# Kernel tuning notes

Hardware: AMD Instinct MI355X
Metric: run time of the kernel (lower is better)

The kernel has to match this reference:

```python
import jax, jax.numpy as jnp
import numpy as np

N_NODES = 200000
N_EDGES = 3200000
F_IN = 128
CH = 32
N_GRAPHS = 1024
N_LABELS = 17


def setup_inputs() -> dict:
    key = jax.random.key(0)
    ks = jax.random.split(key, 16)
    x = jax.random.normal(ks[0], (N_NODES, F_IN), dtype=jnp.float32)
    a_row = jax.random.randint(ks[1], (N_EDGES,), 0, N_NODES, dtype=jnp.int64)
    a_col = jax.random.randint(ks[2], (N_EDGES,), 0, N_NODES, dtype=jnp.int64)
    a_val = jax.random.uniform(ks[3], (N_EDGES,), dtype=jnp.float32)
    seg = jnp.sort(jax.random.randint(ks[4], (N_NODES,), 0, N_GRAPHS, dtype=jnp.int64))
    def glorot(k, fan_in, fan_out):
        lim = np.sqrt(6.0 / (fan_in + fan_out)).astype(np.float32)
        return jax.random.uniform(k, (fan_in, fan_out), dtype=jnp.float32, minval=-lim, maxval=lim)
    params = {
        'W1_1': glorot(ks[5], F_IN, CH), 'W2_1': glorot(ks[6], F_IN, CH), 'b_1': jnp.zeros((CH,), jnp.float32),
        'W1_2': glorot(ks[7], CH, CH),   'W2_2': glorot(ks[8], CH, CH),   'b_2': jnp.zeros((CH,), jnp.float32),
        'W1_3': glorot(ks[9], CH, CH),   'W2_3': glorot(ks[10], CH, CH),  'b_3': jnp.zeros((CH,), jnp.float32),
        'Wd': glorot(ks[11], CH, N_LABELS), 'bd': jnp.zeros((N_LABELS,), jnp.float32),
    }
    return dict(x=x, a_row=a_row, a_col=a_col, a_val=a_val, seg=seg, **params)


def _gcs_conv(x, a_row, a_col, a_val, W1, W2, b):
    # A @ X via gather(col) -> weight -> scatter-add(row)
    msgs = a_val[:, None] * x[a_col]            # [E, F]
    agg = jax.ops.segment_sum(msgs, a_row, num_segments=N_NODES)  # [N, F]
    return jax.nn.relu(agg @ W1 + x @ W2 + b)


def reference(x, a_row, a_col, a_val, seg,
              W1_1, W2_1, b_1, W1_2, W2_2, b_2, W1_3, W2_3, b_3, Wd, bd):
    h = _gcs_conv(x, a_row, a_col, a_val, W1_1, W2_1, b_1)
    h = _gcs_conv(h, a_row, a_col, a_val, W1_2, W2_2, b_2)
    h = _gcs_conv(h, a_row, a_col, a_val, W1_3, W2_3, b_3)
    # GlobalAvgPool over batch index i: segment mean per graph
    sums = jax.ops.segment_sum(h, seg, num_segments=N_GRAPHS)          # [G, CH]
    cnts = jax.ops.segment_sum(jnp.ones((N_NODES,), h.dtype), seg, num_segments=N_GRAPHS)
    pooled = sums / jnp.maximum(cnts, 1.0)[:, None]
    return jax.nn.softmax(pooled @ Wd + bd, axis=-1)
```

## Files before the change

kernel.cpp:

```cpp
#include <hip/hip_runtime.h>
#include <cstdint>

#define N_NODES 200000
#define N_EDGES 3200000
#define F_IN 128
#define CH 32
#define N_GRAPHS 1024
#define N_LABELS 17

#define BROWS 512
#define NBUCK ((N_NODES + BROWS - 1) / BROWS)
#define CAP 10240
#define EPB 8192

typedef unsigned int uint32;
typedef unsigned short u16;

#define TSCALE 16.f

__device__ __forceinline__ u16 f2bf(float f) {
  unsigned int u = __float_as_uint(f);
  u = (u + 0x7FFFu + ((u >> 16) & 1u)) >> 16;
  return (u16)u;
}
__device__ __forceinline__ float bf2f(u16 h) {
  return __uint_as_float(((unsigned int)h) << 16);
}
__device__ __forceinline__ signed char f2q8(float f) {
  float qf = fmaxf(-127.f, fminf(127.f, rintf(f * TSCALE)));
  return (signed char)(int)qf;
}


__global__ __launch_bounds__(256) void k_passA(const int* __restrict__ arow,
                                               const int* __restrict__ acol,
                                               const float* __restrict__ aval,
                                               int* __restrict__ bucketCur,
                                               unsigned long long* __restrict__ records) {
  __shared__ int cnt[NBUCK];
  __shared__ int base[NBUCK];
  int t = threadIdx.x;
  for (int i = t; i < NBUCK; i += 256) cnt[i] = 0;
  __syncthreads();
  int e0 = blockIdx.x * EPB;
  int e1 = e0 + EPB; if (e1 > N_EDGES) e1 = N_EDGES;
  for (int e = e0 + t; e < e1; e += 256) atomicAdd(&cnt[arow[e] >> 9], 1);
  __syncthreads();
  for (int i = t; i < NBUCK; i += 256) {
    int n = cnt[i];
    base[i] = n ? atomicAdd(&bucketCur[i], n) : 0;
    cnt[i] = 0;
  }
  __syncthreads();
  for (int e = e0 + t; e < e1; e += 256) {
    int r = arow[e];
    int b = r >> 9;
    int p = atomicAdd(&cnt[b], 1) + base[b];
    if (p < CAP) {
      unsigned int hi = ((unsigned int)(r & 511) << 18) | (unsigned int)acol[e];
      unsigned long long rec = ((unsigned long long)hi << 32) |
                               (unsigned int)__float_as_int(aval[e]);
      records[(size_t)b * CAP + p] = rec;
    }
  }
}


__global__ __launch_bounds__(512) void k_passB(const int* __restrict__ bucketCur,
                                               const unsigned long long* __restrict__ records,
                                               int2* __restrict__ rowinfo,
                                               uint32* __restrict__ edges) {
  __shared__ int cnt[BROWS];
  __shared__ int sc[BROWS];
  __shared__ int cur[BROWS];
  int b = blockIdx.x;
  int t = threadIdx.x;
  int nrec = bucketCur[b]; if (nrec > CAP) nrec = CAP;
  const unsigned long long* rp = records + (size_t)b * CAP;
  cnt[t] = 0;
  __syncthreads();
  for (int i = t; i < nrec; i += 512) {
    unsigned int hi = (unsigned int)(rp[i] >> 32);
    atomicAdd(&cnt[hi >> 18], 1);
  }
  __syncthreads();
  sc[t] = cnt[t];
  __syncthreads();
  for (int d = 1; d < BROWS; d <<= 1) {
    int v = (t >= d) ? sc[t - d] : 0;
    __syncthreads();
    sc[t] += v;
    __syncthreads();
  }
  int pre = sc[t] - cnt[t];
  cur[t] = pre;
  int r = b * BROWS + t;
  if (r < N_NODES) rowinfo[r] = make_int2(b * CAP + pre, cnt[t]);
  __syncthreads();
  for (int i = t; i < nrec; i += 512) {
    unsigned long long rec = rp[i];
    unsigned int hi = (unsigned int)(rec >> 32);
    int rl = hi >> 18;
    unsigned int col = hi & 0x3FFFFu;
    float val = __int_as_float((int)(unsigned int)rec);
    int q = (int)fmaf(val, 16383.f, 0.5f);
    q = q < 0 ? 0 : (q > 16383 ? 16383 : q);
    int p = atomicAdd(&cur[rl], 1);
    edges[(size_t)b * CAP + p] = (col << 14) | (unsigned int)q;
  }
}


__global__ __launch_bounds__(256) void k_dense1(const float* __restrict__ x,
                                                const float* __restrict__ W1,
                                                const float* __restrict__ W2,
                                                signed char* __restrict__ tout,
                                                u16* __restrict__ sout) {
  int i = blockIdx.x * blockDim.x + threadIdx.x;
  if (i >= N_NODES) return;
  const float* xr = x + (size_t)i * F_IN;
  float acc1[CH], acc2[CH];
#pragma unroll
  for (int c = 0; c < CH; c++) { acc1[c] = 0.f; acc2[c] = 0.f; }
#pragma unroll 8
  for (int k = 0; k < F_IN; k += 4) {
    float4 xv = *(const float4*)(xr + k);
    float xk[4] = {xv.x, xv.y, xv.z, xv.w};
#pragma unroll
    for (int kk = 0; kk < 4; kk++) {
      float xval = xk[kk];
      const float* w1r = W1 + (size_t)(k + kk) * CH;
      const float* w2r = W2 + (size_t)(k + kk) * CH;
#pragma unroll
      for (int c = 0; c < CH; c++) {
        acc1[c] = fmaf(xval, w1r[c], acc1[c]);
        acc2[c] = fmaf(xval, w2r[c], acc2[c]);
      }
    }
  }
  uint32* tp = (uint32*)(tout + (size_t)i * CH);
#pragma unroll
  for (int c = 0; c < CH; c += 4) {
    uint32 p = ((uint32)(unsigned char)f2q8(acc1[c])) |
               ((uint32)(unsigned char)f2q8(acc1[c + 1]) << 8) |
               ((uint32)(unsigned char)f2q8(acc1[c + 2]) << 16) |
               ((uint32)(unsigned char)f2q8(acc1[c + 3]) << 24);
    tp[c >> 2] = p;
  }
  uint32* sp = (uint32*)(sout + (size_t)i * CH);
#pragma unroll
  for (int c = 0; c < CH; c += 2) {
    sp[c >> 1] = (uint32)f2bf(acc2[c]) | ((uint32)f2bf(acc2[c + 1]) << 16);
  }
}


template <int MODE>
__global__ __launch_bounds__(256) void k_gcs(const int2* __restrict__ rowinfo,
                                             const uint32* __restrict__ edges,
                                             const signed char* __restrict__ tin,
                                             u16* __restrict__ sio,
                                             const float* __restrict__ bias,
                                             const float* __restrict__ W1n,
                                             const float* __restrict__ W2n,
                                             signed char* __restrict__ tout,
                                             float* __restrict__ hout) {
  int gid = blockIdx.x * blockDim.x + threadIdx.x;
  int node = gid >> 5;
  int c = gid & 31;
  if (node >= N_NODES) return;
  int2 ri = rowinfo[node];
  const uint32* ep = edges + ri.x;
  int n = ri.y;
  float s = bf2f(sio[((size_t)node << 5) + c]);
  float a0 = 0.f, a1 = 0.f, a2 = 0.f, a3 = 0.f;
  for (int e = 0; e < n; e += 8) {
    int i0 = e + 0, i1 = e + 1, i2 = e + 2, i3 = e + 3;
    int i4 = e + 4, i5 = e + 5, i6 = e + 6, i7 = e + 7;
    uint32 d0 = ep[i0 < n ? i0 : n - 1];
    uint32 d1 = ep[i1 < n ? i1 : n - 1];
    uint32 d2 = ep[i2 < n ? i2 : n - 1];
    uint32 d3 = ep[i3 < n ? i3 : n - 1];
    uint32 d4 = ep[i4 < n ? i4 : n - 1];
    uint32 d5 = ep[i5 < n ? i5 : n - 1];
    uint32 d6 = ep[i6 < n ? i6 : n - 1];
    uint32 d7 = ep[i7 < n ? i7 : n - 1];
    int g0 = (int)tin[((size_t)(d0 >> 14) << 5) + c];
    int g1 = (int)tin[((size_t)(d1 >> 14) << 5) + c];
    int g2 = (int)tin[((size_t)(d2 >> 14) << 5) + c];
    int g3 = (int)tin[((size_t)(d3 >> 14) << 5) + c];
    int g4 = (int)tin[((size_t)(d4 >> 14) << 5) + c];
    int g5 = (int)tin[((size_t)(d5 >> 14) << 5) + c];
    int g6 = (int)tin[((size_t)(d6 >> 14) << 5) + c];
    int g7 = (int)tin[((size_t)(d7 >> 14) << 5) + c];
    float v0 = (i0 < n) ? (float)(d0 & 0x3FFFu) : 0.f;
    float v1 = (i1 < n) ? (float)(d1 & 0x3FFFu) : 0.f;
    float v2 = (i2 < n) ? (float)(d2 & 0x3FFFu) : 0.f;
    float v3 = (i3 < n) ? (float)(d3 & 0x3FFFu) : 0.f;
    float v4 = (i4 < n) ? (float)(d4 & 0x3FFFu) : 0.f;
    float v5 = (i5 < n) ? (float)(d5 & 0x3FFFu) : 0.f;
    float v6 = (i6 < n) ? (float)(d6 & 0x3FFFu) : 0.f;
    float v7 = (i7 < n) ? (float)(d7 & 0x3FFFu) : 0.f;
    a0 = fmaf(v0, (float)g0, a0);
    a1 = fmaf(v1, (float)g1, a1);
    a2 = fmaf(v2, (float)g2, a2);
    a3 = fmaf(v3, (float)g3, a3);
    a0 = fmaf(v4, (float)g4, a0);
    a1 = fmaf(v5, (float)g5, a1);
    a2 = fmaf(v6, (float)g6, a2);
    a3 = fmaf(v7, (float)g7, a3);
  }
  float acc = ((a0 + a1) + (a2 + a3)) * (1.f / (16383.f * TSCALE));
  float h = fmaxf(acc + s + bias[c], 0.f);
  if (MODE == 1) {
    hout[((size_t)node << 5) + c] = h;
  } else {
    float m1 = 0.f, m2 = 0.f;
#pragma unroll
    for (int k = 0; k < CH; k++) {
      float hk = __shfl(h, k, 32);
      m1 = fmaf(hk, W1n[k * CH + c], m1);
      m2 = fmaf(hk, W2n[k * CH + c], m2);
    }
    tout[((size_t)node << 5) + c] = f2q8(m1);
    sio[((size_t)node << 5) + c] = f2bf(m2);
  }
}


__global__ void k_head(const float* __restrict__ h, const int* __restrict__ seg,
                       const float* __restrict__ Wd, const float* __restrict__ bd,
                       float* __restrict__ out) {
  int g = blockIdx.x;
  int t = threadIdx.x;
  __shared__ float red[64];
  __shared__ float pooled[CH];
  __shared__ float logits[N_LABELS];
  int lo, hi;
  {
    int l = 0, r = N_NODES;
    while (l < r) { int m = (l + r) >> 1; if (seg[m] < g) l = m + 1; else r = m; }
    lo = l;
  }
  {
    int l = 0, r = N_NODES;
    while (l < r) { int m = (l + r) >> 1; if (seg[m] < g + 1) l = m + 1; else r = m; }
    hi = l;
  }
  float acc = 0.f;
  int c = t & 31, half = t >> 5;
  for (int i = lo + half; i < hi; i += 2) acc += h[(size_t)i * CH + c];
  red[t] = acc;
  __syncthreads();
  if (t < CH) {
    float cnt = (float)((hi - lo) > 0 ? (hi - lo) : 1);
    pooled[t] = (red[t] + red[t + 32]) / cnt;
  }
  __syncthreads();
  if (t < N_LABELS) {
    float a = bd[t];
#pragma unroll
    for (int k = 0; k < CH; k++) a = fmaf(pooled[k], Wd[k * N_LABELS + t], a);
    logits[t] = a;
  }
  __syncthreads();
  if (t == 0) {
    float mx = logits[0];
    for (int j = 1; j < N_LABELS; j++) mx = fmaxf(mx, logits[j]);
    float ssum = 0.f;
    float e[N_LABELS];
    for (int j = 0; j < N_LABELS; j++) { e[j] = expf(logits[j] - mx); ssum += e[j]; }
    float inv = 1.f / ssum;
    for (int j = 0; j < N_LABELS; j++) out[(size_t)g * N_LABELS + j] = e[j] * inv;
  }
}


extern "C" void kernel_launch(void* const* d_in, const int* in_sizes, int n_in,
                              void* d_out, int out_size, void* d_ws, size_t ws_size,
                              hipStream_t stream) {
  const float* x    = (const float*)d_in[0];
  const int*   arow = (const int*)d_in[1];
  const int*   acol = (const int*)d_in[2];
  const float* aval = (const float*)d_in[3];
  const int*   seg  = (const int*)d_in[4];
  const float* W1_1 = (const float*)d_in[5];
  const float* W2_1 = (const float*)d_in[6];
  const float* b_1  = (const float*)d_in[7];
  const float* W1_2 = (const float*)d_in[8];
  const float* W2_2 = (const float*)d_in[9];
  const float* b_2  = (const float*)d_in[10];
  const float* W1_3 = (const float*)d_in[11];
  const float* W2_3 = (const float*)d_in[12];
  const float* b_3  = (const float*)d_in[13];
  const float* Wd   = (const float*)d_in[14];
  const float* bd   = (const float*)d_in[15];
  float* out = (float*)d_out;

  char* w = (char*)d_ws;
  signed char* tA = (signed char*)w; w += (size_t)N_NODES * CH;
  signed char* tB = (signed char*)w; w += (size_t)N_NODES * CH;
  u16* sS = (u16*)w;                 w += (size_t)N_NODES * CH * 2;
  float* hbuf = (float*)w;           w += (size_t)N_NODES * CH * 4;
  uint32* edges = (uint32*)w;        w += (size_t)NBUCK * CAP * 4;
  int2* rowinfo = (int2*)w;          w += (size_t)N_NODES * 8;
  int* bucketCur = (int*)w;          w += (size_t)NBUCK * 4;
  unsigned long long* records = (unsigned long long*)d_ws;

  hipMemsetAsync(bucketCur, 0, (size_t)NBUCK * 4, stream);
  k_passA<<<(N_EDGES + EPB - 1) / EPB, 256, 0, stream>>>(arow, acol, aval, bucketCur, records);
  k_passB<<<NBUCK, 512, 0, stream>>>(bucketCur, records, rowinfo, edges);

  k_dense1<<<(N_NODES + 255) / 256, 256, 0, stream>>>(x, W1_1, W2_1, tA, sS);

  const int GCS_GRID = (N_NODES * 32 + 255) / 256;
  k_gcs<0><<<GCS_GRID, 256, 0, stream>>>(rowinfo, edges, tA, sS, b_1, W1_2, W2_2, tB, nullptr);
  k_gcs<0><<<GCS_GRID, 256, 0, stream>>>(rowinfo, edges, tB, sS, b_2, W1_3, W2_3, tA, nullptr);
  k_gcs<1><<<GCS_GRID, 256, 0, stream>>>(rowinfo, edges, tA, sS, b_3, nullptr, nullptr, nullptr, hbuf);

  k_head<<<N_GRAPHS, 64, 0, stream>>>(hbuf, seg, Wd, bd, out);
}
```

Before: 414.4 us.

## Transpose input to bf16 k-major layout for coalesced dense layer loads

Adds a kernel that converts x to bf16 and transposes it into a k-major layout of packed feature pairs. The first dense layer then reads one coalesced word per thread per feature pair instead of per-thread strided rows. This targets uncoalesced memory access in the dense pass. In exchange it adds an extra kernel pass over x and lowers input precision to bf16.

```diff
diff --git a/kernel.cpp b/kernel.cpp
--- a/kernel.cpp
+++ b/kernel.cpp
@@ -111,34 +111,71 @@
 }
 
 
-__global__ __launch_bounds__(256) void k_dense1(const float* __restrict__ x,
+__global__ __launch_bounds__(256) void k_xpose(const float* __restrict__ x,
+                                               uint32* __restrict__ xT) {
+  __shared__ u16 tile[64 * 136];
+  int t = threadIdx.x;
+  const float4* x4 = (const float4*)x;
+  size_t base4 = (size_t)blockIdx.x * 2048;
+#pragma unroll
+  for (int j = 0; j < 8; j++) {
+    float4 v = x4[base4 + t + 256 * j];
+    int row = (t >> 5) + 8 * j;
+    int k0 = (t & 31) * 4;
+    ushort4 p;
+    p.x = f2bf(v.x); p.y = f2bf(v.y); p.z = f2bf(v.z); p.w = f2bf(v.w);
+    *(ushort4*)&tile[row * 136 + k0] = p;
+  }
+  __syncthreads();
+  int kp = t & 63;
+  int nq = t >> 6;
+  uint32 o[16];
+#pragma unroll
+  for (int r = 0; r < 16; r++) {
+    int node = nq * 16 + r;
+    o[r] = *(const uint32*)&tile[node * 136 + kp * 2];
+  }
+  uint32* dst = xT + (size_t)kp * N_NODES + blockIdx.x * 64 + nq * 16;
+#pragma unroll
+  for (int r = 0; r < 16; r += 4) {
+    *(uint4*)(dst + r) = make_uint4(o[r], o[r + 1], o[r + 2], o[r + 3]);
+  }
+}
+
+
+__global__ __launch_bounds__(256) void k_dense1(const uint32* __restrict__ xT,
                                                 const float* __restrict__ W1,
                                                 const float* __restrict__ W2,
                                                 signed char* __restrict__ tout,
                                                 u16* __restrict__ sout) {
-  int i = blockIdx.x * blockDim.x + threadIdx.x;
-  if (i >= N_NODES) return;
-  const float* xr = x + (size_t)i * F_IN;
+  int node = blockIdx.x * blockDim.x + threadIdx.x;
+  if (node >= N_NODES) return;
   float acc1[CH], acc2[CH];
 #pragma unroll
   for (int c = 0; c < CH; c++) { acc1[c] = 0.f; acc2[c] = 0.f; }
-#pragma unroll 8
-  for (int k = 0; k < F_IN; k += 4) {
-    float4 xv = *(const float4*)(xr + k);
-    float xk[4] = {xv.x, xv.y, xv.z, xv.w};
-#pragma unroll
-    for (int kk = 0; kk < 4; kk++) {
-      float xval = xk[kk];
-      const float* w1r = W1 + (size_t)(k + kk) * CH;
-      const float* w2r = W2 + (size_t)(k + kk) * CH;
+  for (int kp0 = 0; kp0 < 64; kp0 += 8) {
+    uint32 st[8];
+#pragma unroll
+    for (int i = 0; i < 8; i++) st[i] = xT[(size_t)(kp0 + i) * N_NODES + node];
+#pragma unroll
+    for (int i = 0; i < 8; i++) {
+      float xlo = bf2f((u16)(st[i] & 0xffffu));
+      float xhi = bf2f((u16)(st[i] >> 16));
+      const float* w1lo = W1 + (size_t)(2 * (kp0 + i)) * CH;
+      const float* w2lo = W2 + (size_t)(2 * (kp0 + i)) * CH;
 #pragma unroll
       for (int c = 0; c < CH; c++) {
-        acc1[c] = fmaf(xval, w1r[c], acc1[c]);
-        acc2[c] = fmaf(xval, w2r[c], acc2[c]);
+        acc1[c] = fmaf(xlo, w1lo[c], acc1[c]);
+        acc2[c] = fmaf(xlo, w2lo[c], acc2[c]);
+      }
+#pragma unroll
+      for (int c = 0; c < CH; c++) {
+        acc1[c] = fmaf(xhi, w1lo[CH + c], acc1[c]);
+        acc2[c] = fmaf(xhi, w2lo[CH + c], acc2[c]);
       }
     }
   }
-  uint32* tp = (uint32*)(tout + (size_t)i * CH);
+  uint32* tp = (uint32*)(tout + (size_t)node * CH);
 #pragma unroll
   for (int c = 0; c < CH; c += 4) {
     uint32 p = ((uint32)(unsigned char)f2q8(acc1[c])) |
@@ -147,7 +184,7 @@
                ((uint32)(unsigned char)f2q8(acc1[c + 3]) << 24);
     tp[c >> 2] = p;
   }
-  uint32* sp = (uint32*)(sout + (size_t)i * CH);
+  uint32* sp = (uint32*)(sout + (size_t)node * CH);
 #pragma unroll
   for (int c = 0; c < CH; c += 2) {
     sp[c >> 1] = (uint32)f2bf(acc2[c]) | ((uint32)f2bf(acc2[c + 1]) << 16);
@@ -304,14 +341,17 @@
   float* hbuf = (float*)w;           w += (size_t)N_NODES * CH * 4;
   uint32* edges = (uint32*)w;        w += (size_t)NBUCK * CAP * 4;
   int2* rowinfo = (int2*)w;          w += (size_t)N_NODES * 8;
-  int* bucketCur = (int*)w;          w += (size_t)NBUCK * 4;
+  int* bucketCur = (int*)w;          w += 4096;
+  uint32* xT = (uint32*)w;           w += (size_t)64 * N_NODES * 4;
   unsigned long long* records = (unsigned long long*)d_ws;
 
   hipMemsetAsync(bucketCur, 0, (size_t)NBUCK * 4, stream);
   k_passA<<<(N_EDGES + EPB - 1) / EPB, 256, 0, stream>>>(arow, acol, aval, bucketCur, records);
   k_passB<<<NBUCK, 512, 0, stream>>>(bucketCur, records, rowinfo, edges);
 
-  k_dense1<<<(N_NODES + 255) / 256, 256, 0, stream>>>(x, W1_1, W2_1, tA, sS);
+  k_xpose<<<N_NODES / 64, 256, 0, stream>>>(x, xT);
+
+  k_dense1<<<(N_NODES + 255) / 256, 256, 0, stream>>>(xT, W1_1, W2_1, tA, sS);
 
   const int GCS_GRID = (N_NODES * 32 + 255) / 256;
   k_gcs<0><<<GCS_GRID, 256, 0, stream>>>(rowinfo, edges, tA, sS, b_1, W1_2, W2_2, tB, nullptr);
```

Result: slower. 466.7 us (+12.6%).

## Split channel dimension into halves so each gather table fits in cache

Applied to the files above, without the earlier changes.

The int8 feature table is split into two 16-channel halves (3.2MB each). Each aggregation layer now runs twice over the edge list, once per half, so the randomly gathered table is smaller and more likely to stay in L2/LLC. The channel-mixing matmul moves into a separate k_mix kernel, and the intermediate h is stored as bf16. The cost is reading the edge list twice per layer, extra kernel launches, and an extra round trip of h through memory.

```diff
diff --git a/kernel.cpp b/kernel.cpp
--- a/kernel.cpp
+++ b/kernel.cpp
@@ -114,7 +114,8 @@
 __global__ __launch_bounds__(256) void k_dense1(const float* __restrict__ x,
                                                 const float* __restrict__ W1,
                                                 const float* __restrict__ W2,
-                                                signed char* __restrict__ tout,
+                                                signed char* __restrict__ tlo,
+                                                signed char* __restrict__ thi,
                                                 u16* __restrict__ sout) {
   int i = blockIdx.x * blockDim.x + threadIdx.x;
   if (i >= N_NODES) return;
@@ -138,16 +139,20 @@
       }
     }
   }
-  uint32* tp = (uint32*)(tout + (size_t)i * CH);
-#pragma unroll
-  for (int c = 0; c < CH; c += 4) {
-    uint32 p = ((uint32)(unsigned char)f2q8(acc1[c])) |
-               ((uint32)(unsigned char)f2q8(acc1[c + 1]) << 8) |
-               ((uint32)(unsigned char)f2q8(acc1[c + 2]) << 16) |
-               ((uint32)(unsigned char)f2q8(acc1[c + 3]) << 24);
-    tp[c >> 2] = p;
-  }
-  uint32* sp = (uint32*)(sout + (size_t)i * CH);
+  uint32* tlp = (uint32*)(tlo + ((size_t)i << 4));
+  uint32* thp = (uint32*)(thi + ((size_t)i << 4));
+#pragma unroll
+  for (int c = 0; c < 16; c += 4) {
+    tlp[c >> 2] = ((uint32)(unsigned char)f2q8(acc1[c])) |
+                  ((uint32)(unsigned char)f2q8(acc1[c + 1]) << 8) |
+                  ((uint32)(unsigned char)f2q8(acc1[c + 2]) << 16) |
+                  ((uint32)(unsigned char)f2q8(acc1[c + 3]) << 24);
+    thp[c >> 2] = ((uint32)(unsigned char)f2q8(acc1[16 + c])) |
+                  ((uint32)(unsigned char)f2q8(acc1[16 + c + 1]) << 8) |
+                  ((uint32)(unsigned char)f2q8(acc1[16 + c + 2]) << 16) |
+                  ((uint32)(unsigned char)f2q8(acc1[16 + c + 3]) << 24);
+  }
+  uint32* sp = (uint32*)(sout + ((size_t)i << 5));
 #pragma unroll
   for (int c = 0; c < CH; c += 2) {
     sp[c >> 1] = (uint32)f2bf(acc2[c]) | ((uint32)f2bf(acc2[c + 1]) << 16);
@@ -155,24 +160,20 @@
 }
 
 
-template <int MODE>
-__global__ __launch_bounds__(256) void k_gcs(const int2* __restrict__ rowinfo,
-                                             const uint32* __restrict__ edges,
-                                             const signed char* __restrict__ tin,
-                                             u16* __restrict__ sio,
-                                             const float* __restrict__ bias,
-                                             const float* __restrict__ W1n,
-                                             const float* __restrict__ W2n,
-                                             signed char* __restrict__ tout,
-                                             float* __restrict__ hout) {
+__global__ __launch_bounds__(256) void k_gcsh(const int2* __restrict__ rowinfo,
+                                              const uint32* __restrict__ edges,
+                                              const signed char* __restrict__ tin,
+                                              const u16* __restrict__ sio,
+                                              const float* __restrict__ bias,
+                                              u16* __restrict__ hout, int choff) {
   int gid = blockIdx.x * blockDim.x + threadIdx.x;
-  int node = gid >> 5;
-  int c = gid & 31;
+  int node = gid >> 4;
+  int c = gid & 15;
   if (node >= N_NODES) return;
   int2 ri = rowinfo[node];
   const uint32* ep = edges + ri.x;
   int n = ri.y;
-  float s = bf2f(sio[((size_t)node << 5) + c]);
+  float s = bf2f(sio[((size_t)node << 5) + choff + c]);
   float a0 = 0.f, a1 = 0.f, a2 = 0.f, a3 = 0.f;
   for (int e = 0; e < n; e += 8) {
     int i0 = e + 0, i1 = e + 1, i2 = e + 2, i3 = e + 3;
@@ -185,14 +186,14 @@
     uint32 d5 = ep[i5 < n ? i5 : n - 1];
     uint32 d6 = ep[i6 < n ? i6 : n - 1];
     uint32 d7 = ep[i7 < n ? i7 : n - 1];
-    int g0 = (int)tin[((size_t)(d0 >> 14) << 5) + c];
-    int g1 = (int)tin[((size_t)(d1 >> 14) << 5) + c];
-    int g2 = (int)tin[((size_t)(d2 >> 14) << 5) + c];
-    int g3 = (int)tin[((size_t)(d3 >> 14) << 5) + c];
-    int g4 = (int)tin[((size_t)(d4 >> 14) << 5) + c];
-    int g5 = (int)tin[((size_t)(d5 >> 14) << 5) + c];
-    int g6 = (int)tin[((size_t)(d6 >> 14) << 5) + c];
-    int g7 = (int)tin[((size_t)(d7 >> 14) << 5) + c];
+    int g0 = (int)tin[((size_t)(d0 >> 14) << 4) + c];
+    int g1 = (int)tin[((size_t)(d1 >> 14) << 4) + c];
+    int g2 = (int)tin[((size_t)(d2 >> 14) << 4) + c];
+    int g3 = (int)tin[((size_t)(d3 >> 14) << 4) + c];
+    int g4 = (int)tin[((size_t)(d4 >> 14) << 4) + c];
+    int g5 = (int)tin[((size_t)(d5 >> 14) << 4) + c];
+    int g6 = (int)tin[((size_t)(d6 >> 14) << 4) + c];
+    int g7 = (int)tin[((size_t)(d7 >> 14) << 4) + c];
     float v0 = (i0 < n) ? (float)(d0 & 0x3FFFu) : 0.f;
     float v1 = (i1 < n) ? (float)(d1 & 0x3FFFu) : 0.f;
     float v2 = (i2 < n) ? (float)(d2 & 0x3FFFu) : 0.f;
@@ -211,26 +212,40 @@
     a3 = fmaf(v7, (float)g7, a3);
   }
   float acc = ((a0 + a1) + (a2 + a3)) * (1.f / (16383.f * TSCALE));
-  float h = fmaxf(acc + s + bias[c], 0.f);
-  if (MODE == 1) {
-    hout[((size_t)node << 5) + c] = h;
-  } else {
-    float m1 = 0.f, m2 = 0.f;
-#pragma unroll
-    for (int k = 0; k < CH; k++) {
-      float hk = __shfl(h, k, 32);
-      m1 = fmaf(hk, W1n[k * CH + c], m1);
-      m2 = fmaf(hk, W2n[k * CH + c], m2);
-    }
-    tout[((size_t)node << 5) + c] = f2q8(m1);
-    sio[((size_t)node << 5) + c] = f2bf(m2);
-  }
-}
-
-
-__global__ void k_head(const float* __restrict__ h, const int* __restrict__ seg,
-                       const float* __restrict__ Wd, const float* __restrict__ bd,
-                       float* __restrict__ out) {
+  float h = fmaxf(acc + s + bias[choff + c], 0.f);
+  hout[((size_t)node << 4) + c] = f2bf(h);
+}
+
+
+__global__ __launch_bounds__(256) void k_mix(const u16* __restrict__ hl,
+                                             const u16* __restrict__ hh,
+                                             const float* __restrict__ W1n,
+                                             const float* __restrict__ W2n,
+                                             signed char* __restrict__ tlo,
+                                             signed char* __restrict__ thi,
+                                             u16* __restrict__ sio) {
+  int gid = blockIdx.x * blockDim.x + threadIdx.x;
+  int node = gid >> 5;
+  int c = gid & 31;
+  if (node >= N_NODES) return;
+  const u16* hp = (c < 16) ? hl : hh;
+  float h = bf2f(hp[((size_t)node << 4) + (c & 15)]);
+  float m1 = 0.f, m2 = 0.f;
+#pragma unroll
+  for (int k = 0; k < CH; k++) {
+    float hk = __shfl(h, k, 32);
+    m1 = fmaf(hk, W1n[k * CH + c], m1);
+    m2 = fmaf(hk, W2n[k * CH + c], m2);
+  }
+  signed char* tp = (c < 16) ? tlo : thi;
+  tp[((size_t)node << 4) + (c & 15)] = f2q8(m1);
+  sio[((size_t)node << 5) + c] = f2bf(m2);
+}
+
+
+__global__ void k_head(const u16* __restrict__ hl, const u16* __restrict__ hh,
+                       const int* __restrict__ seg, const float* __restrict__ Wd,
+                       const float* __restrict__ bd, float* __restrict__ out) {
   int g = blockIdx.x;
   int t = threadIdx.x;
   __shared__ float red[64];
@@ -249,7 +264,9 @@
   }
   float acc = 0.f;
   int c = t & 31, half = t >> 5;
-  for (int i = lo + half; i < hi; i += 2) acc += h[(size_t)i * CH + c];
+  const u16* hp = (c < 16) ? hl : hh;
+  int ci = c & 15;
+  for (int i = lo + half; i < hi; i += 2) acc += bf2f(hp[((size_t)i << 4) + ci]);
   red[t] = acc;
   __syncthreads();
   if (t < CH) {
@@ -297,26 +314,38 @@
   const float* bd   = (const float*)d_in[15];
   float* out = (float*)d_out;
 
+  const size_t HALF = (size_t)N_NODES * 16;
+
   char* w = (char*)d_ws;
-  signed char* tA = (signed char*)w; w += (size_t)N_NODES * CH;
-  signed char* tB = (signed char*)w; w += (size_t)N_NODES * CH;
-  u16* sS = (u16*)w;                 w += (size_t)N_NODES * CH * 2;
-  float* hbuf = (float*)w;           w += (size_t)N_NODES * CH * 4;
-  uint32* edges = (uint32*)w;        w += (size_t)NBUCK * CAP * 4;
-  int2* rowinfo = (int2*)w;          w += (size_t)N_NODES * 8;
-  int* bucketCur = (int*)w;          w += (size_t)NBUCK * 4;
+  signed char* tAlo = (signed char*)w; w += HALF;
+  signed char* tAhi = (signed char*)w; w += HALF;
+  signed char* tBlo = (signed char*)w; w += HALF;
+  signed char* tBhi = (signed char*)w; w += HALF;
+  u16* sS = (u16*)w;                   w += (size_t)N_NODES * CH * 2;
+  u16* hL = (u16*)w;                   w += HALF * 2;
+  u16* hH = (u16*)w;                   w += HALF * 2;
+  uint32* edges = (uint32*)w;          w += (size_t)NBUCK * CAP * 4;
+  int2* rowinfo = (int2*)w;            w += (size_t)N_NODES * 8;
+  int* bucketCur = (int*)w;            w += 4096;
   unsigned long long* records = (unsigned long long*)d_ws;
 
   hipMemsetAsync(bucketCur, 0, (size_t)NBUCK * 4, stream);
   k_passA<<<(N_EDGES + EPB - 1) / EPB, 256, 0, stream>>>(arow, acol, aval, bucketCur, records);
   k_passB<<<NBUCK, 512, 0, stream>>>(bucketCur, records, rowinfo, edges);
 
-  k_dense1<<<(N_NODES + 255) / 256, 256, 0, stream>>>(x, W1_1, W2_1, tA, sS);
-
-  const int GCS_GRID = (N_NODES * 32 + 255) / 256;
-  k_gcs<0><<<GCS_GRID, 256, 0, stream>>>(rowinfo, edges, tA, sS, b_1, W1_2, W2_2, tB, nullptr);
-  k_gcs<0><<<GCS_GRID, 256, 0, stream>>>(rowinfo, edges, tB, sS, b_2, W1_3, W2_3, tA, nullptr);
-  k_gcs<1><<<GCS_GRID, 256, 0, stream>>>(rowinfo, edges, tA, sS, b_3, nullptr, nullptr, nullptr, hbuf);
-
-  k_head<<<N_GRAPHS, 64, 0, stream>>>(hbuf, seg, Wd, bd, out);
-}
+  k_dense1<<<(N_NODES + 255) / 256, 256, 0, stream>>>(x, W1_1, W2_1, tAlo, tAhi, sS);
+
+  const int GH_GRID = (N_NODES * 16 + 255) / 256;
+  const int MIX_GRID = (N_NODES * 32 + 255) / 256;
+
+  k_gcsh<<<GH_GRID, 256, 0, stream>>>(rowinfo, edges, tAlo, sS, b_1, hL, 0);
+  k_gcsh<<<GH_GRID, 256, 0, stream>>>(rowinfo, edges, tAhi, sS, b_1, hH, 16);
+  k_mix<<<MIX_GRID, 256, 0, stream>>>(hL, hH, W1_2, W2_2, tBlo, tBhi, sS);
+  k_gcsh<<<GH_GRID, 256, 0, stream>>>(rowinfo, edges, tBlo, sS, b_2, hL, 0);
+  k_gcsh<<<GH_GRID, 256, 0, stream>>>(rowinfo, edges, tBhi, sS, b_2, hH, 16);
+  k_mix<<<MIX_GRID, 256, 0, stream>>>(hL, hH, W1_3, W2_3, tAlo, tAhi, sS);
+  k_gcsh<<<GH_GRID, 256, 0, stream>>>(rowinfo, edges, tAlo, sS, b_3, hL, 0);
+  k_gcsh<<<GH_GRID, 256, 0, stream>>>(rowinfo, edges, tAhi, sS, b_3, hH, 16);
+
+  k_head<<<N_GRAPHS, 64, 0, stream>>>(hL, hH, seg, Wd, bd, out);
+}
```

Result: slower. 458.0 us (+10.5%).

## Merge first dense layer with edge bucketing pass and widen gather unroll

Applied to the files above, without the earlier changes.

Merges the first dense layer and the edge-bucketing pass A into a single launch, with blocks split by index so both run at the same time. Records move to a separate workspace region so pass A no longer overwrites the tA/sS buffers that the dense part writes. The GCS gather loop is also unrolled from 8 to 16 edges per iteration to keep more loads in flight. This costs more registers per thread and extra workspace memory.

```diff
diff --git a/kernel.cpp b/kernel.cpp
--- a/kernel.cpp
+++ b/kernel.cpp
@@ -12,6 +12,8 @@
 #define NBUCK ((N_NODES + BROWS - 1) / BROWS)
 #define CAP 10240
 #define EPB 8192
+#define NB_D1 ((N_NODES + 255) / 256)
+#define NB_A ((N_EDGES + EPB - 1) / EPB)
 
 typedef unsigned int uint32;
 typedef unsigned short u16;
@@ -32,17 +34,63 @@
 }
 
 
-__global__ __launch_bounds__(256) void k_passA(const int* __restrict__ arow,
-                                               const int* __restrict__ acol,
-                                               const float* __restrict__ aval,
-                                               int* __restrict__ bucketCur,
-                                               unsigned long long* __restrict__ records) {
+__global__ __launch_bounds__(256) void k_d1A(const float* __restrict__ x,
+                                             const float* __restrict__ W1,
+                                             const float* __restrict__ W2,
+                                             signed char* __restrict__ tout,
+                                             u16* __restrict__ sout,
+                                             const int* __restrict__ arow,
+                                             const int* __restrict__ acol,
+                                             const float* __restrict__ aval,
+                                             int* __restrict__ bucketCur,
+                                             unsigned long long* __restrict__ records) {
   __shared__ int cnt[NBUCK];
   __shared__ int base[NBUCK];
+  int blk = blockIdx.x;
   int t = threadIdx.x;
+  if (blk < NB_D1) {
+    int i = blk * 256 + t;
+    if (i >= N_NODES) return;
+    const float* xr = x + (size_t)i * F_IN;
+    float acc1[CH], acc2[CH];
+#pragma unroll
+    for (int c = 0; c < CH; c++) { acc1[c] = 0.f; acc2[c] = 0.f; }
+#pragma unroll 8
+    for (int k = 0; k < F_IN; k += 4) {
+      float4 xv = *(const float4*)(xr + k);
+      float xk[4] = {xv.x, xv.y, xv.z, xv.w};
+#pragma unroll
+      for (int kk = 0; kk < 4; kk++) {
+        float xval = xk[kk];
+        const float* w1r = W1 + (size_t)(k + kk) * CH;
+        const float* w2r = W2 + (size_t)(k + kk) * CH;
+#pragma unroll
+        for (int c = 0; c < CH; c++) {
+          acc1[c] = fmaf(xval, w1r[c], acc1[c]);
+          acc2[c] = fmaf(xval, w2r[c], acc2[c]);
+        }
+      }
+    }
+    uint32* tp = (uint32*)(tout + (size_t)i * CH);
+#pragma unroll
+    for (int c = 0; c < CH; c += 4) {
+      uint32 p = ((uint32)(unsigned char)f2q8(acc1[c])) |
+                 ((uint32)(unsigned char)f2q8(acc1[c + 1]) << 8) |
+                 ((uint32)(unsigned char)f2q8(acc1[c + 2]) << 16) |
+                 ((uint32)(unsigned char)f2q8(acc1[c + 3]) << 24);
+      tp[c >> 2] = p;
+    }
+    uint32* sp = (uint32*)(sout + (size_t)i * CH);
+#pragma unroll
+    for (int c = 0; c < CH; c += 2) {
+      sp[c >> 1] = (uint32)f2bf(acc2[c]) | ((uint32)f2bf(acc2[c + 1]) << 16);
+    }
+    return;
+  }
+  int ab = blk - NB_D1;
   for (int i = t; i < NBUCK; i += 256) cnt[i] = 0;
   __syncthreads();
-  int e0 = blockIdx.x * EPB;
+  int e0 = ab * EPB;
   int e1 = e0 + EPB; if (e1 > N_EDGES) e1 = N_EDGES;
   for (int e = e0 + t; e < e1; e += 256) atomicAdd(&cnt[arow[e] >> 9], 1);
   __syncthreads();
@@ -107,50 +155,6 @@
     q = q < 0 ? 0 : (q > 16383 ? 16383 : q);
     int p = atomicAdd(&cur[rl], 1);
     edges[(size_t)b * CAP + p] = (col << 14) | (unsigned int)q;
-  }
-}
-
-
-__global__ __launch_bounds__(256) void k_dense1(const float* __restrict__ x,
-                                                const float* __restrict__ W1,
-                                                const float* __restrict__ W2,
-                                                signed char* __restrict__ tout,
-                                                u16* __restrict__ sout) {
-  int i = blockIdx.x * blockDim.x + threadIdx.x;
-  if (i >= N_NODES) return;
-  const float* xr = x + (size_t)i * F_IN;
-  float acc1[CH], acc2[CH];
-#pragma unroll
-  for (int c = 0; c < CH; c++) { acc1[c] = 0.f; acc2[c] = 0.f; }
-#pragma unroll 8
-  for (int k = 0; k < F_IN; k += 4) {
-    float4 xv = *(const float4*)(xr + k);
-    float xk[4] = {xv.x, xv.y, xv.z, xv.w};
-#pragma unroll
-    for (int kk = 0; kk < 4; kk++) {
-      float xval = xk[kk];
-      const float* w1r = W1 + (size_t)(k + kk) * CH;
-      const float* w2r = W2 + (size_t)(k + kk) * CH;
-#pragma unroll
-      for (int c = 0; c < CH; c++) {
-        acc1[c] = fmaf(xval, w1r[c], acc1[c]);
-        acc2[c] = fmaf(xval, w2r[c], acc2[c]);
-      }
-    }
-  }
-  uint32* tp = (uint32*)(tout + (size_t)i * CH);
-#pragma unroll
-  for (int c = 0; c < CH; c += 4) {
-    uint32 p = ((uint32)(unsigned char)f2q8(acc1[c])) |
-               ((uint32)(unsigned char)f2q8(acc1[c + 1]) << 8) |
-               ((uint32)(unsigned char)f2q8(acc1[c + 2]) << 16) |
-               ((uint32)(unsigned char)f2q8(acc1[c + 3]) << 24);
-    tp[c >> 2] = p;
-  }
-  uint32* sp = (uint32*)(sout + (size_t)i * CH);
-#pragma unroll
-  for (int c = 0; c < CH; c += 2) {
-    sp[c >> 1] = (uint32)f2bf(acc2[c]) | ((uint32)f2bf(acc2[c + 1]) << 16);
   }
 }
 
@@ -173,44 +177,30 @@
   const uint32* ep = edges + ri.x;
   int n = ri.y;
   float s = bf2f(sio[((size_t)node << 5) + c]);
-  float a0 = 0.f, a1 = 0.f, a2 = 0.f, a3 = 0.f;
-  for (int e = 0; e < n; e += 8) {
-    int i0 = e + 0, i1 = e + 1, i2 = e + 2, i3 = e + 3;
-    int i4 = e + 4, i5 = e + 5, i6 = e + 6, i7 = e + 7;
-    uint32 d0 = ep[i0 < n ? i0 : n - 1];
-    uint32 d1 = ep[i1 < n ? i1 : n - 1];
-    uint32 d2 = ep[i2 < n ? i2 : n - 1];
-    uint32 d3 = ep[i3 < n ? i3 : n - 1];
-    uint32 d4 = ep[i4 < n ? i4 : n - 1];
-    uint32 d5 = ep[i5 < n ? i5 : n - 1];
-    uint32 d6 = ep[i6 < n ? i6 : n - 1];
-    uint32 d7 = ep[i7 < n ? i7 : n - 1];
-    int g0 = (int)tin[((size_t)(d0 >> 14) << 5) + c];
-    int g1 = (int)tin[((size_t)(d1 >> 14) << 5) + c];
-    int g2 = (int)tin[((size_t)(d2 >> 14) << 5) + c];
-    int g3 = (int)tin[((size_t)(d3 >> 14) << 5) + c];
-    int g4 = (int)tin[((size_t)(d4 >> 14) << 5) + c];
-    int g5 = (int)tin[((size_t)(d5 >> 14) << 5) + c];
-    int g6 = (int)tin[((size_t)(d6 >> 14) << 5) + c];
-    int g7 = (int)tin[((size_t)(d7 >> 14) << 5) + c];
-    float v0 = (i0 < n) ? (float)(d0 & 0x3FFFu) : 0.f;
-    float v1 = (i1 < n) ? (float)(d1 & 0x3FFFu) : 0.f;
-    float v2 = (i2 < n) ? (float)(d2 & 0x3FFFu) : 0.f;
-    float v3 = (i3 < n) ? (float)(d3 & 0x3FFFu) : 0.f;
-    float v4 = (i4 < n) ? (float)(d4 & 0x3FFFu) : 0.f;
-    float v5 = (i5 < n) ? (float)(d5 & 0x3FFFu) : 0.f;
-    float v6 = (i6 < n) ? (float)(d6 & 0x3FFFu) : 0.f;
-    float v7 = (i7 < n) ? (float)(d7 & 0x3FFFu) : 0.f;
-    a0 = fmaf(v0, (float)g0, a0);
-    a1 = fmaf(v1, (float)g1, a1);
-    a2 = fmaf(v2, (float)g2, a2);
-    a3 = fmaf(v3, (float)g3, a3);
-    a0 = fmaf(v4, (float)g4, a0);
-    a1 = fmaf(v5, (float)g5, a1);
-    a2 = fmaf(v6, (float)g6, a2);
-    a3 = fmaf(v7, (float)g7, a3);
-  }
-  float acc = ((a0 + a1) + (a2 + a3)) * (1.f / (16383.f * TSCALE));
+  float a[4] = {0.f, 0.f, 0.f, 0.f};
+  for (int e = 0; e < n; e += 16) {
+    uint32 d[16];
+    int g[16];
+    float v[16];
+#pragma unroll
+    for (int j = 0; j < 16; j++) {
+      int ij = e + j;
+      d[j] = ep[ij < n ? ij : n - 1];
+    }
+#pragma unroll
+    for (int j = 0; j < 16; j++) {
+      g[j] = (int)tin[((size_t)(d[j] >> 14) << 5) + c];
+    }
+#pragma unroll
+    for (int j = 0; j < 16; j++) {
+      v[j] = (e + j < n) ? (float)(d[j] & 0x3FFFu) : 0.f;
+    }
+#pragma unroll
+    for (int j = 0; j < 16; j++) {
+      a[j & 3] = fmaf(v[j], (float)g[j], a[j & 3]);
+    }
+  }
+  float acc = ((a[0] + a[1]) + (a[2] + a[3])) * (1.f / (16383.f * TSCALE));
   float h = fmaxf(acc + s + bias[c], 0.f);
   if (MODE == 1) {
     hout[((size_t)node << 5) + c] = h;
@@ -304,14 +294,16 @@
   float* hbuf = (float*)w;           w += (size_t)N_NODES * CH * 4;
   uint32* edges = (uint32*)w;        w += (size_t)NBUCK * CAP * 4;
   int2* rowinfo = (int2*)w;          w += (size_t)N_NODES * 8;
-  int* bucketCur = (int*)w;          w += (size_t)NBUCK * 4;
-  unsigned long long* records = (unsigned long long*)d_ws;
+  int* bucketCur = (int*)w;          w += 4096;
+  unsigned long long* records = (unsigned long long*)w;
+  w += (size_t)NBUCK * CAP * 8;
 
   hipMemsetAsync(bucketCur, 0, (size_t)NBUCK * 4, stream);
-  k_passA<<<(N_EDGES + EPB - 1) / EPB, 256, 0, stream>>>(arow, acol, aval, bucketCur, records);
+
+  k_d1A<<<NB_D1 + NB_A, 256, 0, stream>>>(x, W1_1, W2_1, tA, sS,
+                                          arow, acol, aval, bucketCur, records);
+
   k_passB<<<NBUCK, 512, 0, stream>>>(bucketCur, records, rowinfo, edges);
-
-  k_dense1<<<(N_NODES + 255) / 256, 256, 0, stream>>>(x, W1_1, W2_1, tA, sS);
 
   const int GCS_GRID = (N_NODES * 32 + 255) / 256;
   k_gcs<0><<<GCS_GRID, 256, 0, stream>>>(rowinfo, edges, tA, sS, b_1, W1_2, W2_2, tB, nullptr);
```

After: 425.5 us. +2.7%, slower.
